# Performance work log

Measured on AMD Instinct MI355X. Metric: run time of the kernel, lower is better.

Reference implementation:

```python
import jax, jax.numpy as jnp
import numpy as np

BATCH = 16384
IN = 1024
OUT = 1024
SIGMA_MIN = 0.1
SIGMA_MAX = 1.0


def setup_inputs() -> dict:
    key = jax.random.key(0)
    k0, k1, k2, k3 = jax.random.split(key, 4)
    x = jax.random.normal(k0, (BATCH, IN), dtype=jnp.float32)
    # torch init: triu(randn) -> upper-triangular reflector banks
    U = jnp.triu(jax.random.normal(k1, (IN, IN), dtype=jnp.float32))
    V = jnp.triu(jax.random.normal(k2, (OUT, OUT), dtype=jnp.float32))
    p = 0.001 * jax.random.normal(k3, (min(IN, OUT),), dtype=jnp.float32)
    bias = jnp.zeros((OUT,), dtype=jnp.float32)
    return {"x": x, "U": U, "V": V, "p": p, "bias": bias}


def _hprod_step(x, u):
    # u has zeros in its first i entries (triu row i), so the full-vector
    # form equals torch's sliced Hprod on the last k = n - i columns.
    alpha = 2.0 * (x @ u) / jnp.dot(u, u)          # [bs]
    return x - alpha[:, None] * u[None, :], None   # rank-1 update


def reference(x, U, V, p, bias):
    r = (SIGMA_MAX - SIGMA_MIN) / 2.0
    sigma_mean = SIGMA_MIN + r
    # mask enforces torch slice semantics (entries below diag never used)
    Um = U * jnp.triu(jnp.ones_like(U))
    Vm = V * jnp.triu(jnp.ones_like(V))
    # Umultiply: reflectors i = 0 .. n_U-1 in order (sequential recurrence)
    x, _ = jax.lax.scan(_hprod_step, x, Um)
    # Sigma: diagonal scaling (square case IN == OUT)
    sigmas = 2.0 * r * (jax.nn.sigmoid(p) - 0.5) + sigma_mean
    x = x * sigmas[None, :]
    # Vmultiply: reflectors i = n_V-1 .. 0 (reverse order)
    x, _ = jax.lax.scan(_hprod_step, x, Vm[::-1])
    return x + bias
```

## Files before the change

### kernel.cpp

```cpp
#include <hip/hip_runtime.h>
#include <stdint.h>

typedef __attribute__((ext_vector_type(8))) short short8;
typedef __attribute__((ext_vector_type(4))) float f32x4;

#define NN 1024
#define NBATCH 16384
#define ME ((size_t)NN * NN)

__device__ __forceinline__ unsigned short f32_to_bf16_rne(float f) {
  unsigned int u = __float_as_uint(f);
  unsigned int r = (u + 0x7fffu + ((u >> 16) & 1u)) >> 16;
  return (unsigned short)r;
}

__device__ __forceinline__ unsigned int pack2bf(float lo, float hi) {
  return (unsigned int)f32_to_bf16_rne(lo) | ((unsigned int)f32_to_bf16_rne(hi) << 16);
}

__device__ __forceinline__ void split_bf16(float x, unsigned short& h, unsigned short& l) {
  h = f32_to_bf16_rne(x);
  float hf = __uint_as_float((unsigned int)h << 16);
  l = f32_to_bf16_rne(x - hf);
}

__device__ __forceinline__ float allsum64(float x) {
  x += __int_as_float(__builtin_amdgcn_update_dpp(0, __float_as_int(x), 0xB1, 0xF, 0xF, true));
  x += __int_as_float(__builtin_amdgcn_update_dpp(0, __float_as_int(x), 0x4E, 0xF, 0xF, true));
  x += __int_as_float(__builtin_amdgcn_update_dpp(0, __float_as_int(x), 0x141, 0xF, 0xF, true));
  x += __int_as_float(__builtin_amdgcn_update_dpp(0, __float_as_int(x), 0x140, 0xF, 0xF, true));
#if __has_builtin(__builtin_amdgcn_permlane16_swap) && __has_builtin(__builtin_amdgcn_permlane32_swap)
  {
    auto r16 = __builtin_amdgcn_permlane16_swap(__float_as_uint(x), __float_as_uint(x), false, false);
    x = __uint_as_float(r16[0]) + __uint_as_float(r16[1]);
    auto r32 = __builtin_amdgcn_permlane32_swap(__float_as_uint(x), __float_as_uint(x), false, false);
    x = __uint_as_float(r32[0]) + __uint_as_float(r32[1]);
  }
#else
  x += __int_as_float(__builtin_amdgcn_ds_swizzle(__float_as_int(x), 0x401F));
  x += __shfl_xor(x, 32);
#endif
  return x;
}

__global__ __launch_bounds__(256) void prep_kernel(
    const float* __restrict__ U, const float* __restrict__ V,
    const float* __restrict__ p, float* __restrict__ tau_u,
    float* __restrict__ tau_v, float* __restrict__ sigmas) {
  int wave = threadIdx.x >> 6, lane = threadIdx.x & 63;
  int row = blockIdx.x * 4 + wave;
  if (row < 2048) {
    const float* u = (row < NN) ? (U + (size_t)row * NN) : (V + (size_t)(row - NN) * NN);
    float s = 0.f;
#pragma unroll
    for (int t = 0; t < 16; ++t) { float a = u[lane + (t << 6)]; s += a * a; }
    s = allsum64(s);
    if (lane == 0) {
      float tau = 2.0f / s;
      if (row < NN) tau_u[row] = tau;
      else tau_v[row - NN] = tau;
    }
  } else if (row < 2064) {
    int j = ((row - 2048) << 6) + lane;
    float pj = p[j];
    float sg = 1.0f / (1.0f + expf(-pj));
    sigmas[j] = 0.9f * (sg - 0.5f) + 0.55f;
  }
}

__global__ __launch_bounds__(64) void gram_t8_kernel(
    const float* __restrict__ U, const float* __restrict__ V,
    const float* __restrict__ tau_u, const float* __restrict__ tau_v,
    float* __restrict__ T8all) {
  __shared__ float G[64];
  const int blk = blockIdx.x;
  const int lane = threadIdx.x;
  const float* bank;
  int rbase, rsign, st;
  if (blk < 128) { bank = U; rbase = 8 * blk; rsign = 1; st = 8 * blk; }
  else { int s = blk - 128; bank = V; rbase = 1023 - 8 * s; rsign = -1; st = 1016 - 8 * s; }

  if (lane < 28) {
    int j = 1, k = 0, t = lane;
    for (int jj = 1; jj < 8; ++jj) {
      int lo = jj * (jj - 1) / 2, hi = jj * (jj + 1) / 2;
      if (t >= lo && t < hi) { j = jj; k = t - lo; }
    }
    const float* rk = bank + (size_t)(rbase + rsign * k) * NN;
    const float* rj = bank + (size_t)(rbase + rsign * j) * NN;
    float acc = 0.f;
    for (int i = st >> 2; i < 256; ++i) {
      float4 a = *reinterpret_cast<const float4*>(rk + 4 * i);
      float4 b = *reinterpret_cast<const float4*>(rj + 4 * i);
      acc += a.x * b.x + a.y * b.y + a.z * b.z + a.w * b.w;
    }
    G[k * 8 + j] = acc;
  }
  __syncthreads();

  if (lane < 8) {
    float Tr[8];
#pragma unroll
    for (int j = 0; j < 8; ++j) Tr[j] = 0.f;
#pragma unroll
    for (int j = 0; j < 8; ++j) {
      int grow = rbase + rsign * j;
      float tj = (blk < 128) ? tau_u[grow] : tau_v[grow];
      float a = 0.f;
#pragma unroll
      for (int k = 0; k < 8; ++k) {
        if (k < j) a += Tr[k] * G[k * 8 + j];
      }
      Tr[j] = (lane == j) ? tj : (-tj * a);
    }
#pragma unroll
    for (int j = 0; j < 8; ++j) T8all[(size_t)blk * 64 + lane * 8 + j] = Tr[j];
  }
}

__global__ __launch_bounds__(256) void splity_kernel(
    const float* __restrict__ U, const float* __restrict__ V,
    unsigned short* __restrict__ Yhi, unsigned short* __restrict__ Ylo,
    unsigned short* __restrict__ YThi, unsigned short* __restrict__ YTlo) {
  __shared__ float ys[128][129];
  const int tid = threadIdx.x;
  const int c = blockIdx.x >> 3, et = blockIdx.x & 7;
  const int half = tid & 1;
  const int slot = tid >> 1;
  const int e0 = et << 7;
  const int grow = (c < 8) ? ((c << 7) + slot) : (1023 - ((c - 8) << 7) - slot);
  const float* src = ((c < 8) ? U : V) + (size_t)grow * NN + e0 + (half << 6);
#pragma unroll
  for (int i = 0; i < 16; ++i) {
    float4 v4 = *reinterpret_cast<const float4*>(src + (i << 2));
    const int kk = (half << 6) + (i << 2);
    ys[slot][kk + 0] = v4.x; ys[slot][kk + 1] = v4.y;
    ys[slot][kk + 2] = v4.z; ys[slot][kk + 3] = v4.w;
  }
  __syncthreads();
  {
    const size_t rbase = ((size_t)(c * 128 + slot)) * NN + e0 + (half << 6);
#pragma unroll
    for (int i = 0; i < 16; ++i) {
      const int kk = (half << 6) + (i << 2);
      ushort4 h4, l4;
      split_bf16(ys[slot][kk + 0], h4.x, l4.x);
      split_bf16(ys[slot][kk + 1], h4.y, l4.y);
      split_bf16(ys[slot][kk + 2], h4.z, l4.z);
      split_bf16(ys[slot][kk + 3], h4.w, l4.w);
      *reinterpret_cast<ushort4*>(&Yhi[rbase + (i << 2)]) = h4;
      *reinterpret_cast<ushort4*>(&Ylo[rbase + (i << 2)]) = l4;
    }
  }
  {
    const int e = slot;
    const size_t tbase = ((size_t)c * 1024 + e0 + e) * 128 + (half << 6);
#pragma unroll
    for (int i = 0; i < 16; ++i) {
      const int k0 = (half << 6) + (i << 2);
      ushort4 h4, l4;
      split_bf16(ys[k0 + 0][e], h4.x, l4.x);
      split_bf16(ys[k0 + 1][e], h4.y, l4.y);
      split_bf16(ys[k0 + 2][e], h4.z, l4.z);
      split_bf16(ys[k0 + 3][e], h4.w, l4.w);
      *reinterpret_cast<ushort4*>(&YThi[tbase + (i << 2)]) = h4;
      *reinterpret_cast<ushort4*>(&YTlo[tbase + (i << 2)]) = l4;
    }
  }
}

#define LDK 40
#define BM 128
#define BN 128
#define BK 32

__device__ __forceinline__ void tile_compute(
    const unsigned short* __restrict__ As, const unsigned short* __restrict__ Bs,
    f32x4 acc[4][4], int arow0, int brow0, int fr, int kb) {
  short8 af[4], bf[4];
#pragma unroll
  for (int tr = 0; tr < 4; ++tr)
    af[tr] = *reinterpret_cast<const short8*>(&As[(arow0 + tr * 16 + fr) * LDK + kb]);
#pragma unroll
  for (int tc = 0; tc < 4; ++tc)
    bf[tc] = *reinterpret_cast<const short8*>(&Bs[(brow0 + tc * 16 + fr) * LDK + kb]);
#pragma unroll
  for (int tr = 0; tr < 4; ++tr)
#pragma unroll
    for (int tc = 0; tc < 4; ++tc)
      acc[tr][tc] = __builtin_amdgcn_mfma_f32_16x16x32_bf16(af[tr], bf[tc], acc[tr][tc], 0, 0, 0);
}

__global__ __launch_bounds__(256) void gramt_kernel(
    const unsigned short* __restrict__ Yhi, const unsigned short* __restrict__ Ylo,
    float* __restrict__ Gp) {
  __shared__ unsigned short Hs[128 * LDK];
  __shared__ unsigned short Ls[128 * LDK];
  const int tid = threadIdx.x;
  const int lane = tid & 63, wave = tid >> 6;
  const int c = blockIdx.x >> 3, ks = blockIdx.x & 7;
  const int wm = wave & 1, wn = wave >> 1;
  const int srow = tid >> 1, scol = (tid & 1) << 4;
  const unsigned short* ph = Yhi + ((size_t)(c * 128 + srow)) * NN + ks * 128 + scol;
  const unsigned short* pl = Ylo + ((size_t)(c * 128 + srow)) * NN + ks * 128 + scol;

  f32x4 acc[4][4];
#pragma unroll
  for (int a = 0; a < 4; ++a)
#pragma unroll
    for (int b = 0; b < 4; ++b) acc[a][b] = 0.f;

  const int arow0 = wm * 64, brow0 = wn * 64;
  const int fr = lane & 15, kb = (lane >> 4) << 3;

#pragma unroll 1
  for (int kt = 0; kt < 4; ++kt) {
    __syncthreads();
    *reinterpret_cast<uint4*>(&Hs[srow * LDK + scol]) = *reinterpret_cast<const uint4*>(ph + kt * 32);
    *reinterpret_cast<uint4*>(&Hs[srow * LDK + scol + 8]) = *reinterpret_cast<const uint4*>(ph + kt * 32 + 8);
    *reinterpret_cast<uint4*>(&Ls[srow * LDK + scol]) = *reinterpret_cast<const uint4*>(pl + kt * 32);
    *reinterpret_cast<uint4*>(&Ls[srow * LDK + scol + 8]) = *reinterpret_cast<const uint4*>(pl + kt * 32 + 8);
    __syncthreads();
    short8 ah[4], al[4], bh[4], bl[4];
#pragma unroll
    for (int tr = 0; tr < 4; ++tr) {
      ah[tr] = *reinterpret_cast<const short8*>(&Hs[(arow0 + tr * 16 + fr) * LDK + kb]);
      al[tr] = *reinterpret_cast<const short8*>(&Ls[(arow0 + tr * 16 + fr) * LDK + kb]);
    }
#pragma unroll
    for (int tc = 0; tc < 4; ++tc) {
      bh[tc] = *reinterpret_cast<const short8*>(&Hs[(brow0 + tc * 16 + fr) * LDK + kb]);
      bl[tc] = *reinterpret_cast<const short8*>(&Ls[(brow0 + tc * 16 + fr) * LDK + kb]);
    }
#pragma unroll
    for (int tr = 0; tr < 4; ++tr)
#pragma unroll
      for (int tc = 0; tc < 4; ++tc) {
        acc[tr][tc] = __builtin_amdgcn_mfma_f32_16x16x32_bf16(ah[tr], bh[tc], acc[tr][tc], 0, 0, 0);
        acc[tr][tc] = __builtin_amdgcn_mfma_f32_16x16x32_bf16(ah[tr], bl[tc], acc[tr][tc], 0, 0, 0);
        acc[tr][tc] = __builtin_amdgcn_mfma_f32_16x16x32_bf16(al[tr], bh[tc], acc[tr][tc], 0, 0, 0);
      }
  }
  const int rq = (lane >> 4) << 2;
#pragma unroll
  for (int tc = 0; tc < 4; ++tc) {
    const int gc = brow0 + tc * 16 + fr;
#pragma unroll
    for (int tr = 0; tr < 4; ++tr) {
      const int gr = arow0 + tr * 16 + rq;
#pragma unroll
      for (int q = 0; q < 4; ++q)
        Gp[(((size_t)c * 8 + ks) * 128 + gr + q) * 128 + gc] = acc[tr][tc][q];
    }
  }
}

__global__ __launch_bounds__(256) void ttree_kernel(
    const float* __restrict__ Gp, const float* __restrict__ T8all,
    unsigned short* __restrict__ Thi, unsigned short* __restrict__ Tlo) {
  __shared__ float Ts[128 * 128];
  __shared__ float Gb[64 * 64];
  __shared__ float Xb[64 * 64];
  const int c = blockIdx.x, tid = threadIdx.x;
  for (int i = tid; i < 128 * 128; i += 256) Ts[i] = 0.f;
  __syncthreads();
  for (int i = tid; i < 1024; i += 256) {
    const int sb = i >> 6, ij = i & 63, r = ij >> 3, col = ij & 7;
    const int t8i = (c < 8) ? (16 * c + sb) : (128 + 16 * (c - 8) + sb);
    Ts[(8 * sb + r) * 128 + 8 * sb + col] = T8all[(size_t)t8i * 64 + ij];
  }
  __syncthreads();
  for (int b = 8; b <= 64; b <<= 1) {
    const int nm = 128 / (2 * b);
    for (int m = 0; m < nm; ++m) {
      const int a0 = 2 * b * m;
      for (int i = tid; i < b * b; i += 256) {
        const int r = i / b, cl = i % b;
        float s = 0.f;
#pragma unroll
        for (int sl = 0; sl < 8; ++sl)
          s += Gp[(((size_t)c * 8 + sl) * 128 + a0 + r) * 128 + a0 + b + cl];
        Gb[i] = s;
      }
      __syncthreads();
      for (int i = tid; i < b * b; i += 256) {
        const int r = i / b, cl = i % b;
        float s = 0.f;
        for (int k = 0; k <= cl; ++k)
          s += Gb[r * b + k] * Ts[(a0 + b + k) * 128 + a0 + b + cl];
        Xb[i] = s;
      }
      __syncthreads();
      for (int i = tid; i < b * b; i += 256) {
        const int r = i / b, cl = i % b;
        float s = 0.f;
        for (int k = r; k < b; ++k)
          s -= Ts[(a0 + r) * 128 + a0 + k] * Xb[k * b + cl];
        Ts[(a0 + r) * 128 + a0 + b + cl] = s;
      }
      __syncthreads();
    }
  }
  for (int i = tid; i < 128 * 128; i += 256) {
    unsigned short h, l;
    split_bf16(Ts[i], h, l);
    Thi[(size_t)c * 128 * 128 + i] = h;
    Tlo[(size_t)c * 128 * 128 + i] = l;
  }
}

__global__ __launch_bounds__(256) void zw_kernel(
    const unsigned short* __restrict__ Thi, const unsigned short* __restrict__ Tlo,
    const unsigned short* __restrict__ YThi, const unsigned short* __restrict__ YTlo,
    unsigned short* __restrict__ WThi, unsigned short* __restrict__ WTlo) {
  __shared__ unsigned short Xh[128 * LDK], Xl[128 * LDK];
  __shared__ unsigned short Wh[128 * LDK], Wl[128 * LDK];
  const int tid = threadIdx.x;
  const int lane = tid & 63, wave = tid >> 6;
  const int c = blockIdx.x >> 3, bn = blockIdx.x & 7;
  const int n0 = bn * 128;
  const int wm = wave & 1, wn = wave >> 1;
  const int srow = tid >> 1, scol = (tid & 1) << 4;
  const unsigned short* pxh = Thi + ((size_t)c * 128 + srow) * 128 + scol;
  const unsigned short* pxl = Tlo + ((size_t)c * 128 + srow) * 128 + scol;
  const unsigned short* pwh = YThi + ((size_t)c * 1024 + n0 + srow) * 128 + scol;
  const unsigned short* pwl = YTlo + ((size_t)c * 1024 + n0 + srow) * 128 + scol;

  f32x4 acc[4][4];
#pragma unroll
  for (int a = 0; a < 4; ++a)
#pragma unroll
    for (int b = 0; b < 4; ++b) acc[a][b] = 0.f;

  const int arow0 = wm * 64, brow0 = wn * 64;
  const int fr = lane & 15, kb = (lane >> 4) << 3;

#pragma unroll 1
  for (int kt = 0; kt < 4; ++kt) {
    __syncthreads();
    *reinterpret_cast<uint4*>(&Xh[srow * LDK + scol]) = *reinterpret_cast<const uint4*>(pxh + kt * 32);
    *reinterpret_cast<uint4*>(&Xh[srow * LDK + scol + 8]) = *reinterpret_cast<const uint4*>(pxh + kt * 32 + 8);
    *reinterpret_cast<uint4*>(&Xl[srow * LDK + scol]) = *reinterpret_cast<const uint4*>(pxl + kt * 32);
    *reinterpret_cast<uint4*>(&Xl[srow * LDK + scol + 8]) = *reinterpret_cast<const uint4*>(pxl + kt * 32 + 8);
    *reinterpret_cast<uint4*>(&Wh[srow * LDK + scol]) = *reinterpret_cast<const uint4*>(pwh + kt * 32);
    *reinterpret_cast<uint4*>(&Wh[srow * LDK + scol + 8]) = *reinterpret_cast<const uint4*>(pwh + kt * 32 + 8);
    *reinterpret_cast<uint4*>(&Wl[srow * LDK + scol]) = *reinterpret_cast<const uint4*>(pwl + kt * 32);
    *reinterpret_cast<uint4*>(&Wl[srow * LDK + scol + 8]) = *reinterpret_cast<const uint4*>(pwl + kt * 32 + 8);
    __syncthreads();
    short8 ah[4], al[4], bh[4], bl[4];
#pragma unroll
    for (int tr = 0; tr < 4; ++tr) {
      ah[tr] = *reinterpret_cast<const short8*>(&Xh[(arow0 + tr * 16 + fr) * LDK + kb]);
      al[tr] = *reinterpret_cast<const short8*>(&Xl[(arow0 + tr * 16 + fr) * LDK + kb]);
    }
#pragma unroll
    for (int tc = 0; tc < 4; ++tc) {
      bh[tc] = *reinterpret_cast<const short8*>(&Wh[(brow0 + tc * 16 + fr) * LDK + kb]);
      bl[tc] = *reinterpret_cast<const short8*>(&Wl[(brow0 + tc * 16 + fr) * LDK + kb]);
    }
#pragma unroll
    for (int tr = 0; tr < 4; ++tr)
#pragma unroll
      for (int tc = 0; tc < 4; ++tc) {
        acc[tr][tc] = __builtin_amdgcn_mfma_f32_16x16x32_bf16(ah[tr], bh[tc], acc[tr][tc], 0, 0, 0);
        acc[tr][tc] = __builtin_amdgcn_mfma_f32_16x16x32_bf16(ah[tr], bl[tc], acc[tr][tc], 0, 0, 0);
        acc[tr][tc] = __builtin_amdgcn_mfma_f32_16x16x32_bf16(al[tr], bh[tc], acc[tr][tc], 0, 0, 0);
      }
  }
  const int rq = (lane >> 4) << 2;
#pragma unroll
  for (int tc = 0; tc < 4; ++tc) {
    const int gc = brow0 + tc * 16 + fr;
#pragma unroll
    for (int tr = 0; tr < 4; ++tr) {
      const int gr = arow0 + tr * 16 + rq;
      ushort4 h4, l4;
      split_bf16(acc[tr][tc][0], h4.x, l4.x);
      split_bf16(acc[tr][tc][1], h4.y, l4.y);
      split_bf16(acc[tr][tc][2], h4.z, l4.z);
      split_bf16(acc[tr][tc][3], h4.w, l4.w);
      const size_t off = ((size_t)c * 1024 + n0 + gc) * 128 + gr;
      *reinterpret_cast<ushort4*>(&WThi[off]) = h4;
      *reinterpret_cast<ushort4*>(&WTlo[off]) = l4;
    }
  }
}

__global__ __launch_bounds__(256) void chainc_kernel(
    const unsigned short* __restrict__ YThi, const unsigned short* __restrict__ YTlo,
    const unsigned short* __restrict__ WThi, const unsigned short* __restrict__ WTlo,
    unsigned short* __restrict__ chains) {
  __shared__ unsigned short Xh[128 * LDK], Xl[128 * LDK];
  __shared__ unsigned short Wh[128 * LDK], Wl[128 * LDK];
  const int tid = threadIdx.x;
  const int lane = tid & 63, wave = tid >> 6;
  const int c = blockIdx.x >> 6, b6 = blockIdx.x & 63;
  const int bm = b6 & 7, bn = b6 >> 3;
  const int m0 = bm * 128, n0 = bn * 128;
  const int wm = wave & 1, wn = wave >> 1;
  const int srow = tid >> 1, scol = (tid & 1) << 4;
  const unsigned short* pxh = YThi + ((size_t)c * 1024 + m0 + srow) * 128 + scol;
  const unsigned short* pxl = YTlo + ((size_t)c * 1024 + m0 + srow) * 128 + scol;
  const unsigned short* pwh = WThi + ((size_t)c * 1024 + n0 + srow) * 128 + scol;
  const unsigned short* pwl = WTlo + ((size_t)c * 1024 + n0 + srow) * 128 + scol;

  f32x4 acc[4][4];
#pragma unroll
  for (int a = 0; a < 4; ++a)
#pragma unroll
    for (int b = 0; b < 4; ++b) acc[a][b] = 0.f;

  const int arow0 = wm * 64, brow0 = wn * 64;
  const int fr = lane & 15, kb = (lane >> 4) << 3;

#pragma unroll 1
  for (int kt = 0; kt < 4; ++kt) {
    __syncthreads();
    *reinterpret_cast<uint4*>(&Xh[srow * LDK + scol]) = *reinterpret_cast<const uint4*>(pxh + kt * 32);
    *reinterpret_cast<uint4*>(&Xh[srow * LDK + scol + 8]) = *reinterpret_cast<const uint4*>(pxh + kt * 32 + 8);
    *reinterpret_cast<uint4*>(&Xl[srow * LDK + scol]) = *reinterpret_cast<const uint4*>(pxl + kt * 32);
    *reinterpret_cast<uint4*>(&Xl[srow * LDK + scol + 8]) = *reinterpret_cast<const uint4*>(pxl + kt * 32 + 8);
    *reinterpret_cast<uint4*>(&Wh[srow * LDK + scol]) = *reinterpret_cast<const uint4*>(pwh + kt * 32);
    *reinterpret_cast<uint4*>(&Wh[srow * LDK + scol + 8]) = *reinterpret_cast<const uint4*>(pwh + kt * 32 + 8);
    *reinterpret_cast<uint4*>(&Wl[srow * LDK + scol]) = *reinterpret_cast<const uint4*>(pwl + kt * 32);
    *reinterpret_cast<uint4*>(&Wl[srow * LDK + scol + 8]) = *reinterpret_cast<const uint4*>(pwl + kt * 32 + 8);
    __syncthreads();
    short8 ah[4], al[4], bh[4], bl[4];
#pragma unroll
    for (int tr = 0; tr < 4; ++tr) {
      ah[tr] = *reinterpret_cast<const short8*>(&Xh[(arow0 + tr * 16 + fr) * LDK + kb]);
      al[tr] = *reinterpret_cast<const short8*>(&Xl[(arow0 + tr * 16 + fr) * LDK + kb]);
    }
#pragma unroll
    for (int tc = 0; tc < 4; ++tc) {
      bh[tc] = *reinterpret_cast<const short8*>(&Wh[(brow0 + tc * 16 + fr) * LDK + kb]);
      bl[tc] = *reinterpret_cast<const short8*>(&Wl[(brow0 + tc * 16 + fr) * LDK + kb]);
    }
#pragma unroll
    for (int tr = 0; tr < 4; ++tr)
#pragma unroll
      for (int tc = 0; tc < 4; ++tc) {
        acc[tr][tc] = __builtin_amdgcn_mfma_f32_16x16x32_bf16(ah[tr], bh[tc], acc[tr][tc], 0, 0, 0);
        acc[tr][tc] = __builtin_amdgcn_mfma_f32_16x16x32_bf16(ah[tr], bl[tc], acc[tr][tc], 0, 0, 0);
        acc[tr][tc] = __builtin_amdgcn_mfma_f32_16x16x32_bf16(al[tr], bh[tc], acc[tr][tc], 0, 0, 0);
      }
  }
  unsigned short* dst = chains + (size_t)c * ME;
  const int rq = (lane >> 4) << 2;
  if ((c & 1) == 0) {
#pragma unroll
    for (int tc = 0; tc < 4; ++tc) {
      const int gcg = n0 + brow0 + tc * 16 + fr;
#pragma unroll
      for (int tr = 0; tr < 4; ++tr) {
        const int grg = m0 + arow0 + tr * 16 + rq;
#pragma unroll
        for (int q = 0; q < 4; ++q) {
          const float val = ((grg + q) == gcg ? 1.0f : 0.0f) - acc[tr][tc][q];
          dst[(size_t)(grg + q) * NN + gcg] = f32_to_bf16_rne(val);
        }
      }
    }
  } else {
#pragma unroll
    for (int tc = 0; tc < 4; ++tc) {
      const int gcg = n0 + brow0 + tc * 16 + fr;
#pragma unroll
      for (int tr = 0; tr < 4; ++tr) {
        const int grg = m0 + arow0 + tr * 16 + rq;
        ushort4 pk;
        pk.x = f32_to_bf16_rne(((grg + 0) == gcg ? 1.0f : 0.0f) - acc[tr][tc][0]);
        pk.y = f32_to_bf16_rne(((grg + 1) == gcg ? 1.0f : 0.0f) - acc[tr][tc][1]);
        pk.z = f32_to_bf16_rne(((grg + 2) == gcg ? 1.0f : 0.0f) - acc[tr][tc][2]);
        pk.w = f32_to_bf16_rne(((grg + 3) == gcg ? 1.0f : 0.0f) - acc[tr][tc][3]);
        *reinterpret_cast<ushort4*>(&dst[(size_t)gcg * NN + grg]) = pk;
      }
    }
  }
}

__device__ __forceinline__ void stage_bf16_tile(
    const unsigned short* __restrict__ gbase, unsigned short* __restrict__ lds,
    int tid, int kt) {
#pragma unroll
  for (int i = 0; i < 2; ++i) {
    const int slot = tid + 256 * i;
    const int row = slot >> 2, s = slot & 3;
    const int cs = s ^ ((row >> 1) & 3);
    __builtin_amdgcn_global_load_lds(
        (const __attribute__((address_space(1))) void*)(gbase + (size_t)row * NN + kt * 32 + cs * 8),
        (__attribute__((address_space(3))) void*)(lds + row * 32 + s * 8), 16, 0, 0);
  }
}

__device__ __forceinline__ void tile_compute32(
    const unsigned short* __restrict__ As, const unsigned short* __restrict__ Bs,
    f32x4 acc[4][4], int arow0, int brow0, int fr, int kb) {
  short8 af[4], bf[4];
  const int ck = kb >> 3;
#pragma unroll
  for (int tr = 0; tr < 4; ++tr) {
    const int row = arow0 + tr * 16 + fr;
    const int sl = ck ^ ((row >> 1) & 3);
    af[tr] = *reinterpret_cast<const short8*>(&As[row * 32 + sl * 8]);
  }
#pragma unroll
  for (int tc = 0; tc < 4; ++tc) {
    const int row = brow0 + tc * 16 + fr;
    const int sl = ck ^ ((row >> 1) & 3);
    bf[tc] = *reinterpret_cast<const short8*>(&Bs[row * 32 + sl * 8]);
  }
#pragma unroll
  for (int tr = 0; tr < 4; ++tr)
#pragma unroll
    for (int tc = 0; tc < 4; ++tc)
      acc[tr][tc] = __builtin_amdgcn_mfma_f32_16x16x32_bf16(af[tr], bf[tc], acc[tr][tc], 0, 0, 0);
}

__device__ __forceinline__ void compose_body(
    const unsigned short* __restrict__ Xb, const unsigned short* __restrict__ Wb,
    unsigned short* __restrict__ Op, const float* __restrict__ sig, int b, bool tstore) {
  __shared__ unsigned short As[2][BM * 32];
  __shared__ unsigned short Bs[2][BN * 32];
  const int tid = threadIdx.x;
  const int lane = tid & 63, wave = tid >> 6;
  const int bm = b & 7, bn = b >> 3;
  const int m0 = bm * BM, n0 = bn * BN;
  const int wm = wave & 1, wn = wave >> 1;
  const int arow0 = wm * 64, brow0 = wn * 64;
  const int fr = lane & 15, kb = (lane >> 4) << 3;

  f32x4 acc[4][4];
#pragma unroll
  for (int a = 0; a < 4; ++a)
#pragma unroll
    for (int bb = 0; bb < 4; ++bb) acc[a][bb] = 0.f;

  const unsigned short* agbase = Xb + (size_t)m0 * NN;
  const unsigned short* bgbase = Wb + (size_t)n0 * NN;

  stage_bf16_tile(agbase, &As[0][0], tid, 0);
  stage_bf16_tile(bgbase, &Bs[0][0], tid, 0);
  int pb = 0;
#pragma unroll 1
  for (int kt = 0; kt < 32; ++kt) {
    __syncthreads();
    if (kt + 1 < 32) {
      stage_bf16_tile(agbase, &As[pb ^ 1][0], tid, kt + 1);
      stage_bf16_tile(bgbase, &Bs[pb ^ 1][0], tid, kt + 1);
    }
    tile_compute32(&As[pb][0], &Bs[pb][0], acc, arow0, brow0, fr, kb);
    pb ^= 1;
  }

  const int rq = (lane >> 4) << 2;
  if (!tstore) {
#pragma unroll
    for (int tc = 0; tc < 4; ++tc) {
      const int gc = n0 + brow0 + tc * 16 + fr;
      const float s = sig ? sig[gc] : 1.0f;
#pragma unroll
      for (int tr = 0; tr < 4; ++tr) {
        const int gr = m0 + arow0 + tr * 16 + rq;
#pragma unroll
        for (int q = 0; q < 4; ++q) {
          Op[(size_t)(gr + q) * NN + gc] = f32_to_bf16_rne(acc[tr][tc][q] * s);
        }
      }
    }
  } else {
#pragma unroll
    for (int tc = 0; tc < 4; ++tc) {
      const int gc = n0 + brow0 + tc * 16 + fr;
#pragma unroll
      for (int tr = 0; tr < 4; ++tr) {
        const int gr = m0 + arow0 + tr * 16 + rq;
        ushort4 pk;
        pk.x = f32_to_bf16_rne(acc[tr][tc][0]);
        pk.y = f32_to_bf16_rne(acc[tr][tc][1]);
        pk.z = f32_to_bf16_rne(acc[tr][tc][2]);
        pk.w = f32_to_bf16_rne(acc[tr][tc][3]);
        *reinterpret_cast<ushort4*>(&Op[(size_t)gc * NN + gr]) = pk;
      }
    }
  }
}

__global__ __launch_bounds__(256) void composeL1_kernel(
    const unsigned short* __restrict__ ch, unsigned short* __restrict__ P) {
  const int sub = blockIdx.x >> 6, b = blockIdx.x & 63;
  const int i = sub & 3;
  const unsigned short* x = ch + (size_t)((sub < 4 ? 0 : 8) + 2 * i) * ME;
  compose_body(x, x + ME, P + (size_t)sub * ME, nullptr, b, (i & 1) != 0);
}

__global__ __launch_bounds__(256) void composeL2_kernel(
    const unsigned short* __restrict__ P, unsigned short* __restrict__ Q) {
  const int sub = blockIdx.x >> 6, b = blockIdx.x & 63;
  compose_body(P + (size_t)(2 * sub) * ME, P + (size_t)(2 * sub + 1) * ME,
               Q + (size_t)sub * ME, nullptr, b, (sub & 1) != 0);
}

__global__ __launch_bounds__(256) void composeL3_kernel(
    const unsigned short* __restrict__ Q, const float* __restrict__ sigmas,
    unsigned short* __restrict__ F) {
  const int sub = blockIdx.x >> 6, b = blockIdx.x & 63;
  if (sub == 0) compose_body(Q, Q + ME, F, sigmas, b, false);
  else compose_body(Q + 2 * ME, Q + 3 * ME, F + ME, nullptr, b, true);
}

__global__ __launch_bounds__(256) void composeL4_kernel(
    const unsigned short* __restrict__ F, unsigned short* __restrict__ Mt) {
  compose_body(F + ME, F, Mt, nullptr, blockIdx.x, false);
}

__global__ __launch_bounds__(256) void gemm_kernel(
    const float* __restrict__ X, const unsigned short* __restrict__ Mt,
    const float* __restrict__ bias, float* __restrict__ Out) {
  __shared__ float Af[2][BM * 32];
  __shared__ unsigned short Bs[2][BN * 32];
  const int tid = threadIdx.x;
  const int lane = tid & 63, wave = tid >> 6;
  const int bm = blockIdx.x & 127;
  const int bn = blockIdx.x >> 7;
  const int m0 = bm * BM, n0 = bn * BN;
  const int wm = wave & 1, wn = wave >> 1;
  const int arow0 = wm * 64, brow0 = wn * 64;
  const int fr = lane & 15, kb = (lane >> 4) << 3;

  f32x4 acc[4][4];
#pragma unroll
  for (int a = 0; a < 4; ++a)
#pragma unroll
    for (int b = 0; b < 4; ++b) acc[a][b] = 0.f;

  const float* agbase = X + (size_t)m0 * NN;
  const unsigned short* bgbase = Mt + (size_t)n0 * NN;

#define GSTAGE(PB, KT)                                                          \
  {                                                                             \
    _Pragma("unroll")                                                           \
    for (int i = 0; i < 4; ++i) {                                               \
      const int slot = tid + 256 * i;                                           \
      const int row = slot >> 3, s = slot & 7;                                  \
      const int cs = s ^ (row & 7);                                             \
      __builtin_amdgcn_global_load_lds(                                         \
          (const __attribute__((address_space(1))) void*)(agbase + (size_t)row * NN + (KT) * 32 + cs * 4), \
          (__attribute__((address_space(3))) void*)(&Af[PB][row * 32 + s * 4]), 16, 0, 0); \
    }                                                                           \
    stage_bf16_tile(bgbase, &Bs[PB][0], tid, KT);                               \
  }

  GSTAGE(0, 0)
  int pb = 0;
#pragma unroll 1
  for (int kt = 0; kt < 32; ++kt) {
    __syncthreads();
    if (kt + 1 < 32) GSTAGE(pb ^ 1, kt + 1)
    {
      short8 af[4], bf[4];
      const int c0 = kb >> 2;
      const int ckb = kb >> 3;
#pragma unroll
      for (int tr = 0; tr < 4; ++tr) {
        const int row = arow0 + tr * 16 + fr;
        const int s0 = c0 ^ (row & 7), s1 = (c0 + 1) ^ (row & 7);
        const f32x4 a0 = *reinterpret_cast<const f32x4*>(&Af[pb][row * 32 + s0 * 4]);
        const f32x4 a1 = *reinterpret_cast<const f32x4*>(&Af[pb][row * 32 + s1 * 4]);
        uint4 w;
        w.x = pack2bf(a0[0], a0[1]); w.y = pack2bf(a0[2], a0[3]);
        w.z = pack2bf(a1[0], a1[1]); w.w = pack2bf(a1[2], a1[3]);
        af[tr] = *reinterpret_cast<const short8*>(&w);
      }
#pragma unroll
      for (int tc = 0; tc < 4; ++tc) {
        const int row = brow0 + tc * 16 + fr;
        const int sl = ckb ^ ((row >> 1) & 3);
        bf[tc] = *reinterpret_cast<const short8*>(&Bs[pb][row * 32 + sl * 8]);
      }
#pragma unroll
      for (int tr = 0; tr < 4; ++tr)
#pragma unroll
        for (int tc = 0; tc < 4; ++tc)
          acc[tr][tc] = __builtin_amdgcn_mfma_f32_16x16x32_bf16(af[tr], bf[tc], acc[tr][tc], 0, 0, 0);
    }
    pb ^= 1;
  }
#undef GSTAGE

  const int rq = (lane >> 4) << 2;
#pragma unroll
  for (int tc = 0; tc < 4; ++tc) {
    const int gc = n0 + brow0 + tc * 16 + fr;
    const float bv = bias[gc];
#pragma unroll
    for (int tr = 0; tr < 4; ++tr) {
      const int gr = m0 + arow0 + tr * 16 + rq;
#pragma unroll
      for (int q = 0; q < 4; ++q) {
        Out[(size_t)(gr + q) * NN + gc] = acc[tr][tc][q] + bv;
      }
    }
  }
}

extern "C" void kernel_launch(void* const* d_in, const int* in_sizes, int n_in,
                              void* d_out, int out_size, void* d_ws, size_t ws_size,
                              hipStream_t stream) {
  const float* x = (const float*)d_in[0];
  const float* U = (const float*)d_in[1];
  const float* V = (const float*)d_in[2];
  const float* p = (const float*)d_in[3];
  const float* bias = (const float*)d_in[4];
  float* out = (float*)d_out;

  char* ws = (char*)d_ws;
  float* tau_u = (float*)(ws);
  float* tau_v = (float*)(ws + 4096);
  float* sigmas = (float*)(ws + 8192);
  float* T8all = (float*)(ws + 16384);
  unsigned short* Mt = (unsigned short*)(ws + 81920);

  unsigned short* sc = (unsigned short*)d_out;
  unsigned short* chains = sc;
  unsigned short* P = sc + 16 * ME;
  unsigned short* Q = sc + 24 * ME;
  unsigned short* F = sc + 28 * ME;
  unsigned short* YThi = sc + 16 * ME;
  unsigned short* YTlo = sc + 18 * ME;
  unsigned short* WThi = sc + 20 * ME;
  unsigned short* WTlo = sc + 22 * ME;
  unsigned short* Yhi = sc + 24 * ME;
  unsigned short* Ylo = sc + 26 * ME;
  float* Gp = (float*)(sc + 28 * ME);
  unsigned short* Thi = sc + 24 * ME;
  unsigned short* Tlo = Thi + 262144;

  prep_kernel<<<516, 256, 0, stream>>>(U, V, p, tau_u, tau_v, sigmas);
  gram_t8_kernel<<<256, 64, 0, stream>>>(U, V, tau_u, tau_v, T8all);
  splity_kernel<<<128, 256, 0, stream>>>(U, V, Yhi, Ylo, YThi, YTlo);
  gramt_kernel<<<128, 256, 0, stream>>>(Yhi, Ylo, Gp);
  ttree_kernel<<<16, 256, 0, stream>>>(Gp, T8all, Thi, Tlo);
  zw_kernel<<<128, 256, 0, stream>>>(Thi, Tlo, YThi, YTlo, WThi, WTlo);
  chainc_kernel<<<1024, 256, 0, stream>>>(YThi, YTlo, WThi, WTlo, chains);
  composeL1_kernel<<<512, 256, 0, stream>>>(chains, P);
  composeL2_kernel<<<256, 256, 0, stream>>>(P, Q);
  composeL3_kernel<<<128, 256, 0, stream>>>(Q, sigmas, F);
  composeL4_kernel<<<64, 256, 0, stream>>>(F, Mt);
  gemm_kernel<<<1024, 256, 0, stream>>>(x, Mt, bias, out);
}
```

Measured before the change: 347.1 us.

## Pre-cast x to bf16, use 256-row GEMM tiles and triple-buffered LDS pipelines

```diff
diff --git a/kernel.cpp b/kernel.cpp
--- a/kernel.cpp
+++ b/kernel.cpp
@@ -7,6 +7,8 @@
 #define NN 1024
 #define NBATCH 16384
 #define ME ((size_t)NN * NN)
+#define AS1 (const __attribute__((address_space(1))) void*)
+#define AS3 (__attribute__((address_space(3))) void*)
 
 __device__ __forceinline__ unsigned short f32_to_bf16_rne(float f) {
   unsigned int u = __float_as_uint(f);
@@ -65,6 +67,18 @@
     float pj = p[j];
     float sg = 1.0f / (1.0f + expf(-pj));
     sigmas[j] = 0.9f * (sg - 0.5f) + 0.55f;
+  }
+}
+
+__global__ __launch_bounds__(256) void castx_kernel(
+    const float* __restrict__ X, unsigned short* __restrict__ Xb) {
+  const size_t n4 = (size_t)NBATCH * NN / 4;
+  for (size_t i = (size_t)blockIdx.x * 256 + threadIdx.x; i < n4; i += (size_t)gridDim.x * 256) {
+    float4 v = reinterpret_cast<const float4*>(X)[i];
+    uint2 o;
+    o.x = pack2bf(v.x, v.y);
+    o.y = pack2bf(v.z, v.w);
+    reinterpret_cast<uint2*>(Xb)[i] = o;
   }
 }
 
@@ -173,23 +187,6 @@
 #define BM 128
 #define BN 128
 #define BK 32
-
-__device__ __forceinline__ void tile_compute(
-    const unsigned short* __restrict__ As, const unsigned short* __restrict__ Bs,
-    f32x4 acc[4][4], int arow0, int brow0, int fr, int kb) {
-  short8 af[4], bf[4];
-#pragma unroll
-  for (int tr = 0; tr < 4; ++tr)
-    af[tr] = *reinterpret_cast<const short8*>(&As[(arow0 + tr * 16 + fr) * LDK + kb]);
-#pragma unroll
-  for (int tc = 0; tc < 4; ++tc)
-    bf[tc] = *reinterpret_cast<const short8*>(&Bs[(brow0 + tc * 16 + fr) * LDK + kb]);
-#pragma unroll
-  for (int tr = 0; tr < 4; ++tr)
-#pragma unroll
-    for (int tc = 0; tc < 4; ++tc)
-      acc[tr][tc] = __builtin_amdgcn_mfma_f32_16x16x32_bf16(af[tr], bf[tc], acc[tr][tc], 0, 0, 0);
-}
 
 __global__ __launch_bounds__(256) void gramt_kernel(
     const unsigned short* __restrict__ Yhi, const unsigned short* __restrict__ Ylo,
@@ -479,37 +476,35 @@
   }
 }
 
-__device__ __forceinline__ void stage_bf16_tile(
-    const unsigned short* __restrict__ gbase, unsigned short* __restrict__ lds,
-    int tid, int kt) {
+__device__ __forceinline__ void cb_stage(
+    const unsigned short* __restrict__ agbase, const unsigned short* __restrict__ bgbase,
+    unsigned short* __restrict__ la, unsigned short* __restrict__ lb, int tid, int kt) {
 #pragma unroll
   for (int i = 0; i < 2; ++i) {
     const int slot = tid + 256 * i;
     const int row = slot >> 2, s = slot & 3;
-    const int cs = s ^ ((row >> 1) & 3);
     __builtin_amdgcn_global_load_lds(
-        (const __attribute__((address_space(1))) void*)(gbase + (size_t)row * NN + kt * 32 + cs * 8),
-        (__attribute__((address_space(3))) void*)(lds + row * 32 + s * 8), 16, 0, 0);
-  }
-}
-
-__device__ __forceinline__ void tile_compute32(
+        AS1(agbase + (size_t)row * NN + kt * 32 + s * 8), AS3(la + row * 32 + s * 8), 16, 0, 0);
+  }
+#pragma unroll
+  for (int i = 0; i < 2; ++i) {
+    const int slot = tid + 256 * i;
+    const int row = slot >> 2, s = slot & 3;
+    __builtin_amdgcn_global_load_lds(
+        AS1(bgbase + (size_t)row * NN + kt * 32 + s * 8), AS3(lb + row * 32 + s * 8), 16, 0, 0);
+  }
+}
+
+__device__ __forceinline__ void cb_compute(
     const unsigned short* __restrict__ As, const unsigned short* __restrict__ Bs,
     f32x4 acc[4][4], int arow0, int brow0, int fr, int kb) {
   short8 af[4], bf[4];
-  const int ck = kb >> 3;
-#pragma unroll
-  for (int tr = 0; tr < 4; ++tr) {
-    const int row = arow0 + tr * 16 + fr;
-    const int sl = ck ^ ((row >> 1) & 3);
-    af[tr] = *reinterpret_cast<const short8*>(&As[row * 32 + sl * 8]);
-  }
-#pragma unroll
-  for (int tc = 0; tc < 4; ++tc) {
-    const int row = brow0 + tc * 16 + fr;
-    const int sl = ck ^ ((row >> 1) & 3);
-    bf[tc] = *reinterpret_cast<const short8*>(&Bs[row * 32 + sl * 8]);
-  }
+#pragma unroll
+  for (int tr = 0; tr < 4; ++tr)
+    af[tr] = *reinterpret_cast<const short8*>(&As[(arow0 + tr * 16 + fr) * 32 + kb]);
+#pragma unroll
+  for (int tc = 0; tc < 4; ++tc)
+    bf[tc] = *reinterpret_cast<const short8*>(&Bs[(brow0 + tc * 16 + fr) * 32 + kb]);
 #pragma unroll
   for (int tr = 0; tr < 4; ++tr)
 #pragma unroll
@@ -520,8 +515,8 @@
 __device__ __forceinline__ void compose_body(
     const unsigned short* __restrict__ Xb, const unsigned short* __restrict__ Wb,
     unsigned short* __restrict__ Op, const float* __restrict__ sig, int b, bool tstore) {
-  __shared__ unsigned short As[2][BM * 32];
-  __shared__ unsigned short Bs[2][BN * 32];
+  __shared__ unsigned short As[3][BM * 32];
+  __shared__ unsigned short Bs[3][BN * 32];
   const int tid = threadIdx.x;
   const int lane = tid & 63, wave = tid >> 6;
   const int bm = b & 7, bn = b >> 3;
@@ -539,19 +534,23 @@
   const unsigned short* agbase = Xb + (size_t)m0 * NN;
   const unsigned short* bgbase = Wb + (size_t)n0 * NN;
 
-  stage_bf16_tile(agbase, &As[0][0], tid, 0);
-  stage_bf16_tile(bgbase, &Bs[0][0], tid, 0);
-  int pb = 0;
+  cb_stage(agbase, bgbase, &As[0][0], &Bs[0][0], tid, 0);
+  cb_stage(agbase, bgbase, &As[1][0], &Bs[1][0], tid, 1);
 #pragma unroll 1
-  for (int kt = 0; kt < 32; ++kt) {
-    __syncthreads();
-    if (kt + 1 < 32) {
-      stage_bf16_tile(agbase, &As[pb ^ 1][0], tid, kt + 1);
-      stage_bf16_tile(bgbase, &Bs[pb ^ 1][0], tid, kt + 1);
-    }
-    tile_compute32(&As[pb][0], &Bs[pb][0], acc, arow0, brow0, fr, kb);
-    pb ^= 1;
-  }
+  for (int kt = 0; kt < 31; ++kt) {
+    asm volatile("s_waitcnt vmcnt(4)" ::: "memory");
+    __builtin_amdgcn_s_barrier();
+    __builtin_amdgcn_sched_barrier(0);
+    if (kt + 2 < 32) {
+      const int nb = (kt + 2) % 3;
+      cb_stage(agbase, bgbase, &As[nb][0], &Bs[nb][0], tid, kt + 2);
+    }
+    cb_compute(&As[kt % 3][0], &Bs[kt % 3][0], acc, arow0, brow0, fr, kb);
+  }
+  asm volatile("s_waitcnt vmcnt(0)" ::: "memory");
+  __builtin_amdgcn_s_barrier();
+  __builtin_amdgcn_sched_barrier(0);
+  cb_compute(&As[1][0], &Bs[1][0], acc, arow0, brow0, fr, kb);
 
   const int rq = (lane >> 4) << 2;
   if (!tstore) {
@@ -614,11 +613,103 @@
   compose_body(F + ME, F, Mt, nullptr, blockIdx.x, false);
 }
 
-__global__ __launch_bounds__(256) void gemm_kernel(
+__global__ __launch_bounds__(512) void gemm256_kernel(
+    const unsigned short* __restrict__ Xb, const unsigned short* __restrict__ Mt,
+    const float* __restrict__ bias, float* __restrict__ Out) {
+  __shared__ unsigned short As[3][256 * 32];
+  __shared__ unsigned short Bs[3][128 * 32];
+  const int tid = threadIdx.x;
+  const int lane = tid & 63, wave = tid >> 6;
+  const int bm = blockIdx.x & 63, bn = blockIdx.x >> 6;
+  const int m0 = bm * 256, n0 = bn * 128;
+  const int wm = wave & 3, wn = wave >> 2;
+  const int arow0 = wm * 64, brow0 = wn * 64;
+  const int fr = lane & 15, kb = (lane >> 4) << 3;
+
+  f32x4 acc[4][4];
+#pragma unroll
+  for (int a = 0; a < 4; ++a)
+#pragma unroll
+    for (int b = 0; b < 4; ++b) acc[a][b] = 0.f;
+
+  const unsigned short* agbase = Xb + (size_t)m0 * NN;
+  const unsigned short* bgbase = Mt + (size_t)n0 * NN;
+
+#define G256_STAGE(B, KT)                                                        \
+  {                                                                              \
+    _Pragma("unroll")                                                            \
+    for (int i = 0; i < 2; ++i) {                                                \
+      const int slot = tid + 512 * i;                                            \
+      const int row = slot >> 2, s = slot & 3;                                   \
+      __builtin_amdgcn_global_load_lds(                                          \
+          AS1(agbase + (size_t)row * NN + (KT) * 32 + s * 8),                    \
+          AS3(&As[B][row * 32 + s * 8]), 16, 0, 0);                              \
+    }                                                                            \
+    {                                                                            \
+      const int row = tid >> 2, s = tid & 3;                                     \
+      __builtin_amdgcn_global_load_lds(                                          \
+          AS1(bgbase + (size_t)row * NN + (KT) * 32 + s * 8),                    \
+          AS3(&Bs[B][row * 32 + s * 8]), 16, 0, 0);                              \
+    }                                                                            \
+  }
+
+#define G256_CMP(B)                                                              \
+  {                                                                              \
+    short8 af[4], bf4[4];                                                        \
+    _Pragma("unroll")                                                            \
+    for (int tr = 0; tr < 4; ++tr)                                               \
+      af[tr] = *reinterpret_cast<const short8*>(&As[B][(arow0 + tr * 16 + fr) * 32 + kb]); \
+    _Pragma("unroll")                                                            \
+    for (int tc = 0; tc < 4; ++tc)                                               \
+      bf4[tc] = *reinterpret_cast<const short8*>(&Bs[B][(brow0 + tc * 16 + fr) * 32 + kb]); \
+    _Pragma("unroll")                                                            \
+    for (int tr = 0; tr < 4; ++tr)                                               \
+      _Pragma("unroll")                                                          \
+      for (int tc = 0; tc < 4; ++tc)                                             \
+        acc[tr][tc] = __builtin_amdgcn_mfma_f32_16x16x32_bf16(af[tr], bf4[tc], acc[tr][tc], 0, 0, 0); \
+  }
+
+  G256_STAGE(0, 0)
+  G256_STAGE(1, 1)
+#pragma unroll 1
+  for (int kt = 0; kt < 31; ++kt) {
+    asm volatile("s_waitcnt vmcnt(3)" ::: "memory");
+    __builtin_amdgcn_s_barrier();
+    __builtin_amdgcn_sched_barrier(0);
+    if (kt + 2 < 32) {
+      const int nb = (kt + 2) % 3;
+      G256_STAGE(nb, kt + 2)
+    }
+    G256_CMP(kt % 3)
+  }
+  asm volatile("s_waitcnt vmcnt(0)" ::: "memory");
+  __builtin_amdgcn_s_barrier();
+  __builtin_amdgcn_sched_barrier(0);
+  G256_CMP(1)
+#undef G256_STAGE
+#undef G256_CMP
+
+  const int rq = (lane >> 4) << 2;
+#pragma unroll
+  for (int tc = 0; tc < 4; ++tc) {
+    const int gc = n0 + brow0 + tc * 16 + fr;
+    const float bv = bias[gc];
+#pragma unroll
+    for (int tr = 0; tr < 4; ++tr) {
+      const int gr = m0 + arow0 + tr * 16 + rq;
+#pragma unroll
+      for (int q = 0; q < 4; ++q) {
+        Out[(size_t)(gr + q) * NN + gc] = acc[tr][tc][q] + bv;
+      }
+    }
+  }
+}
+
+__global__ __launch_bounds__(256) void gemm_fb_kernel(
     const float* __restrict__ X, const unsigned short* __restrict__ Mt,
     const float* __restrict__ bias, float* __restrict__ Out) {
   __shared__ float Af[2][BM * 32];
-  __shared__ unsigned short Bs[2][BN * 32];
+  __shared__ unsigned short Bsl[2][BN * 32];
   const int tid = threadIdx.x;
   const int lane = tid & 63, wave = tid >> 6;
   const int bm = blockIdx.x & 127;
@@ -637,36 +728,40 @@
   const float* agbase = X + (size_t)m0 * NN;
   const unsigned short* bgbase = Mt + (size_t)n0 * NN;
 
-#define GSTAGE(PB, KT)                                                          \
+#define FB_STAGE(PB, KT)                                                        \
   {                                                                             \
     _Pragma("unroll")                                                           \
     for (int i = 0; i < 4; ++i) {                                               \
       const int slot = tid + 256 * i;                                           \
       const int row = slot >> 3, s = slot & 7;                                  \
-      const int cs = s ^ (row & 7);                                             \
       __builtin_amdgcn_global_load_lds(                                         \
-          (const __attribute__((address_space(1))) void*)(agbase + (size_t)row * NN + (KT) * 32 + cs * 4), \
-          (__attribute__((address_space(3))) void*)(&Af[PB][row * 32 + s * 4]), 16, 0, 0); \
+          AS1(agbase + (size_t)row * NN + (KT) * 32 + s * 4),                   \
+          AS3(&Af[PB][row * 32 + s * 4]), 16, 0, 0);                            \
     }                                                                           \
-    stage_bf16_tile(bgbase, &Bs[PB][0], tid, KT);                               \
-  }
-
-  GSTAGE(0, 0)
+    _Pragma("unroll")                                                           \
+    for (int i = 0; i < 2; ++i) {                                               \
+      const int slot = tid + 256 * i;                                           \
+      const int row = slot >> 2, s = slot & 3;                                  \
+      __builtin_amdgcn_global_load_lds(                                         \
+          AS1(bgbase + (size_t)row * NN + (KT) * 32 + s * 8),                   \
+          AS3(&Bsl[PB][row * 32 + s * 8]), 16, 0, 0);                           \
+    }                                                                           \
+  }
+
+  FB_STAGE(0, 0)
   int pb = 0;
 #pragma unroll 1
   for (int kt = 0; kt < 32; ++kt) {
     __syncthreads();
-    if (kt + 1 < 32) GSTAGE(pb ^ 1, kt + 1)
+    if (kt + 1 < 32) FB_STAGE(pb ^ 1, kt + 1)
     {
       short8 af[4], bf[4];
       const int c0 = kb >> 2;
-      const int ckb = kb >> 3;
 #pragma unroll
       for (int tr = 0; tr < 4; ++tr) {
         const int row = arow0 + tr * 16 + fr;
-        const int s0 = c0 ^ (row & 7), s1 = (c0 + 1) ^ (row & 7);
-        const f32x4 a0 = *reinterpret_cast<const f32x4*>(&Af[pb][row * 32 + s0 * 4]);
-        const f32x4 a1 = *reinterpret_cast<const f32x4*>(&Af[pb][row * 32 + s1 * 4]);
+        const f32x4 a0 = *reinterpret_cast<const f32x4*>(&Af[pb][row * 32 + c0 * 4]);
+        const f32x4 a1 = *reinterpret_cast<const f32x4*>(&Af[pb][row * 32 + (c0 + 1) * 4]);
         uint4 w;
         w.x = pack2bf(a0[0], a0[1]); w.y = pack2bf(a0[2], a0[3]);
         w.z = pack2bf(a1[0], a1[1]); w.w = pack2bf(a1[2], a1[3]);
@@ -675,8 +770,7 @@
 #pragma unroll
       for (int tc = 0; tc < 4; ++tc) {
         const int row = brow0 + tc * 16 + fr;
-        const int sl = ckb ^ ((row >> 1) & 3);
-        bf[tc] = *reinterpret_cast<const short8*>(&Bs[pb][row * 32 + sl * 8]);
+        bf[tc] = *reinterpret_cast<const short8*>(&Bsl[pb][row * 32 + kb]);
       }
 #pragma unroll
       for (int tr = 0; tr < 4; ++tr)
@@ -686,7 +780,7 @@
     }
     pb ^= 1;
   }
-#undef GSTAGE
+#undef FB_STAGE
 
   const int rq = (lane >> 4) << 2;
 #pragma unroll
@@ -720,6 +814,11 @@
   float* sigmas = (float*)(ws + 8192);
   float* T8all = (float*)(ws + 16384);
   unsigned short* Mt = (unsigned short*)(ws + 81920);
+
+  const size_t XB_OFF = 4u * 1024 * 1024;
+  const size_t XB_BYTES = (size_t)NBATCH * NN * 2;
+  const bool fast = ws_size >= XB_OFF + XB_BYTES;
+  unsigned short* Xb = (unsigned short*)(ws + XB_OFF);
 
   unsigned short* sc = (unsigned short*)d_out;
   unsigned short* chains = sc;
@@ -737,6 +836,7 @@
   unsigned short* Tlo = Thi + 262144;
 
   prep_kernel<<<516, 256, 0, stream>>>(U, V, p, tau_u, tau_v, sigmas);
+  if (fast) castx_kernel<<<2048, 256, 0, stream>>>(x, Xb);
   gram_t8_kernel<<<256, 64, 0, stream>>>(U, V, tau_u, tau_v, T8all);
   splity_kernel<<<128, 256, 0, stream>>>(U, V, Yhi, Ylo, YThi, YTlo);
   gramt_kernel<<<128, 256, 0, stream>>>(Yhi, Ylo, Gp);
@@ -747,5 +847,6 @@
   composeL2_kernel<<<256, 256, 0, stream>>>(P, Q);
   composeL3_kernel<<<128, 256, 0, stream>>>(Q, sigmas, F);
   composeL4_kernel<<<64, 256, 0, stream>>>(F, Mt);
-  gemm_kernel<<<1024, 256, 0, stream>>>(x, Mt, bias, out);
-}
+  if (fast) gemm256_kernel<<<512, 512, 0, stream>>>(Xb, Mt, bias, out);
+  else gemm_fb_kernel<<<1024, 256, 0, stream>>>(x, Mt, bias, out);
+}
```

Measured after the change: 335.5 us. 1.03x faster.
